# Optimization experiments

Measured on AMD Instinct MI355X. Metric: run time of the kernel, lower is better.

## Reference

```python
import jax, jax.numpy as jnp
import numpy as np

B, L, D, H = 4, 2048, 1024, 16
HD = D // H
EPS = 1e-6
THETA = 10000.0


def _rmsnorm(x, w):
    rms = jax.lax.rsqrt(jnp.mean(x * x, axis=-1, keepdims=True) + EPS)
    return x * rms * w


def _rope(q, k):
    # q,k: [B,H,L,HD]; standard half-split rotary embedding
    pos = jnp.arange(L, dtype=jnp.float32)
    inv_freq = 1.0 / (THETA ** (jnp.arange(0, HD, 2, dtype=jnp.float32) / HD))  # [HD/2]
    ang = pos[:, None] * inv_freq[None, :]                 # [L, HD/2]
    cos = jnp.cos(ang)[None, None]                         # [1,1,L,HD/2]
    sin = jnp.sin(ang)[None, None]

    def rot(t):
        t1, t2 = t[..., : HD // 2], t[..., HD // 2 :]
        return jnp.concatenate([t1 * cos - t2 * sin, t1 * sin + t2 * cos], axis=-1)

    return rot(q), rot(k)


def setup_inputs() -> dict:
    key = jax.random.key(0)
    ks = jax.random.split(key, 4)
    return {
        "x": jax.random.normal(ks[0], (B, L, D), dtype=jnp.float32),
        "Wqkv": jax.random.normal(ks[1], (D, 3 * D), dtype=jnp.float32) * (D ** -0.5),
        "bqkv": jnp.zeros((3 * D,), dtype=jnp.float32),
        "qn_w": jnp.ones((HD,), dtype=jnp.float32),
        "kn_w": jnp.ones((HD,), dtype=jnp.float32),
        "Wout": jax.random.normal(ks[2], (D, D), dtype=jnp.float32) * (D ** -0.5),
        "bout": jnp.zeros((D,), dtype=jnp.float32),
    }


def reference(x, Wqkv, bqkv, qn_w, kn_w, Wout, bout):
    # QKV projection: [B,L,3D] -> [3,B,H,L,HD]
    qkv = (x @ Wqkv + bqkv).reshape(B, L, 3, H, HD).transpose(2, 0, 3, 1, 4)
    q, k, v = qkv[0], qkv[1], qkv[2]
    # QK-RMSNorm over head_dim
    q = _rmsnorm(q, qn_w)
    k = _rmsnorm(k, kn_w)
    # RoPE
    q, k = _rope(q, k)
    # softmax attention
    scale = HD ** -0.5
    attn = jnp.einsum("bhqd,bhkd->bhqk", q, k) * scale
    attn = jax.nn.softmax(attn, axis=-1)
    out = jnp.einsum("bhqk,bhkd->bhqd", attn, v)
    out = out.transpose(0, 2, 1, 3).reshape(B, L, D)
    return out @ Wout + bout
```

## Files before the change

### kernel.cpp

```cpp
#include <hip/hip_runtime.h>
#include <hip/hip_bf16.h>
#include <math.h>


#define NB 4
#define NL 2048
#define ND 1024
#define NH 16
#define NHD 64
#define GM (NB * NL)

typedef _Float16 f16;
typedef _Float16 half4v __attribute__((ext_vector_type(4)));
typedef _Float16 half8v __attribute__((ext_vector_type(8)));
typedef float f32x4 __attribute__((ext_vector_type(4)));

#define MFMA16(a, b, c) __builtin_amdgcn_mfma_f32_16x16x32_f16((a), (b), (c), 0, 0, 0)

__device__ __forceinline__ void gload16(const void* g, void* l) {
  __builtin_amdgcn_global_load_lds((const __attribute__((address_space(1))) void*)g,
                                   (__attribute__((address_space(3))) void*)l, 16, 0, 0);
}

__global__ __launch_bounds__(256) void sctable(float* __restrict__ tbl) {
  const int idx = blockIdx.x * 256 + threadIdx.x;
  const int l = idx >> 5, i = idx & 31;
  const float invf = exp2f(-(float)i * 0.41524101186092029f);
  const float ang = (float)l * invf;
  tbl[idx] = cosf(ang);
  tbl[65536 + idx] = sinf(ang);
}

__global__ __launch_bounds__(256) void transplit(const float* __restrict__ Wsrc,
                                                 f16* __restrict__ Th,
                                                 f16* __restrict__ Tl, int N) {
  __shared__ float t[64][65];
  const int tid = threadIdx.x;
  const int n0 = blockIdx.x * 64, k0 = blockIdx.y * 64;
#pragma unroll
  for (int it = 0; it < 4; ++it) {
    const int e = it * 256 + tid;
    const int r = e >> 4, c4 = (e & 15) << 2;
    const float4 v = *(const float4*)&Wsrc[(size_t)(k0 + r) * N + n0 + c4];
    t[r][c4] = v.x; t[r][c4 + 1] = v.y; t[r][c4 + 2] = v.z; t[r][c4 + 3] = v.w;
  }
  __syncthreads();
#pragma unroll
  for (int it = 0; it < 4; ++it) {
    const int e = it * 256 + tid;
    const int rn = e >> 4, ck = (e & 15) << 2;
    half4v h, lo;
#pragma unroll
    for (int u = 0; u < 4; ++u) {
      const float v = t[ck + u][rn];
      const f16 hv = (f16)v;
      h[u] = hv;
      lo[u] = (f16)(v - (float)hv);
    }
    *(half4v*)&Th[(size_t)(n0 + rn) * 1024 + k0 + ck] = h;
    *(half4v*)&Tl[(size_t)(n0 + rn) * 1024 + k0 + ck] = lo;
  }
}

template <int N, int ASRC, int MODE>
__global__ __launch_bounds__(256) void gemm_split(
    const float* __restrict__ A32, const f16* __restrict__ Ah_g,
    const f16* __restrict__ Al_g, const f16* __restrict__ Bh_g,
    const f16* __restrict__ Bl_g, const float* __restrict__ bias,
    float* __restrict__ out32, f16* __restrict__ qh, f16* __restrict__ ql,
    f16* __restrict__ kh, f16* __restrict__ kl, f16* __restrict__ vth,
    const float* __restrict__ qw, const float* __restrict__ kw,
    const float* __restrict__ tbl) {
  __shared__ f16 Ah[4096], Al[4096], Bh[4096], Bl[4096];
  const int tid = threadIdx.x;
  const int ln = tid & 63, wv = tid >> 6;
  const int ln15 = ln & 15, q4 = ln >> 4;

  const int nwg = (N / 128) * (GM / 128);
  const int flat = blockIdx.y * gridDim.x + blockIdx.x;
  const int sw = (flat & 7) * (nwg >> 3) + (flat >> 3);
  const int bx = sw % (N / 128), by = sw / (N / 128);
  const int m0 = by * 128, n0 = bx * 128;
  const int wr = wv >> 1, wc = wv & 1;

  f32x4 acc[4][4];
#pragma unroll
  for (int i = 0; i < 4; ++i)
#pragma unroll
    for (int j = 0; j < 4; ++j) acc[i][j] = (f32x4){0.f, 0.f, 0.f, 0.f};

  for (int k0 = 0; k0 < 1024; k0 += 32) {
    if constexpr (ASRC == 0) {
#pragma unroll
      for (int it = 0; it < 4; ++it) {
        const int e = it * 256 + tid;
        const int row = e >> 3, kq = (e & 7) << 2;
        const float4 v = *(const float4*)&A32[(size_t)(m0 + row) * 1024 + k0 + kq];
        half4v h, lo;
        h[0] = (f16)v.x; lo[0] = (f16)(v.x - (float)h[0]);
        h[1] = (f16)v.y; lo[1] = (f16)(v.y - (float)h[1]);
        h[2] = (f16)v.z; lo[2] = (f16)(v.z - (float)h[2]);
        h[3] = (f16)v.w; lo[3] = (f16)(v.w - (float)h[3]);
        const int idx = ((row >> 4) << 9) + (((row & 15) + ((kq >> 3) << 4)) << 3) + (kq & 7);
        *(half4v*)&Ah[idx] = h;
        *(half4v*)&Al[idx] = lo;
      }
#pragma unroll
      for (int t = 0; t < 2; ++t) {
        const int f = wv * 2 + t;
        const size_t off = (size_t)(n0 + f * 16 + ln15) * 1024 + k0 + q4 * 8;
        gload16(Bh_g + off, &Bh[f * 512]);
        gload16(Bl_g + off, &Bl[f * 512]);
      }
    } else {
#pragma unroll
      for (int t = 0; t < 2; ++t) {
        const int f = wv * 2 + t;
        const size_t aoff = (size_t)(m0 + f * 16 + ln15) * 1024 + k0 + q4 * 8;
        const size_t boff = (size_t)(n0 + f * 16 + ln15) * 1024 + k0 + q4 * 8;
        gload16(Ah_g + aoff, &Ah[f * 512]);
        gload16(Al_g + aoff, &Al[f * 512]);
        gload16(Bh_g + boff, &Bh[f * 512]);
        gload16(Bl_g + boff, &Bl[f * 512]);
      }
    }
    __syncthreads();

    half8v a_h[4], a_l[4];
#pragma unroll
    for (int i = 0; i < 4; ++i) {
      a_h[i] = *(half8v*)&Ah[(wr * 4 + i) * 512 + ln * 8];
      a_l[i] = *(half8v*)&Al[(wr * 4 + i) * 512 + ln * 8];
    }
#pragma unroll
    for (int j = 0; j < 4; ++j) {
      const half8v b_h = *(half8v*)&Bh[(wc * 4 + j) * 512 + ln * 8];
      const half8v b_l = *(half8v*)&Bl[(wc * 4 + j) * 512 + ln * 8];
#pragma unroll
      for (int i = 0; i < 4; ++i) {
        acc[i][j] = MFMA16(a_h[i], b_h, acc[i][j]);
        acc[i][j] = MFMA16(a_l[i], b_h, acc[i][j]);
        acc[i][j] = MFMA16(a_h[i], b_l, acc[i][j]);
      }
    }
    __syncthreads();
  }

  const int nc = n0 + wc * 64;
  float bv[4];
#pragma unroll
  for (int j = 0; j < 4; ++j) bv[j] = bias[nc + j * 16 + ln15];

  if constexpr (MODE == 0) {
#pragma unroll
    for (int i = 0; i < 4; ++i) {
      const int m = m0 + wr * 64 + i * 16 + q4 * 4;
#pragma unroll
      for (int j = 0; j < 4; ++j)
#pragma unroll
        for (int r = 0; r < 4; ++r)
          out32[(size_t)(m + r) * N + nc + j * 16 + ln15] = acc[i][j][r] + bv[j];
    }
  } else {
    const int s = nc >> 10;
    const int h = (nc >> 6) & 15;
    if (s == 2) {
#pragma unroll
      for (int i = 0; i < 4; ++i) {
        const int m = m0 + wr * 64 + i * 16 + q4 * 4;
        const int b = m >> 11, l0 = m & (NL - 1);
#pragma unroll
        for (int j = 0; j < 4; ++j) {
          half4v pv;
#pragma unroll
          for (int r = 0; r < 4; ++r) pv[r] = (f16)(acc[i][j][r] + bv[j]);
          *(half4v*)&vth[(size_t)((b * NH + h) * NHD + j * 16 + ln15) * NL + l0] = pv;
        }
      }
    } else {
      const float* nw = (s == 0) ? qw : kw;
      f16* dh = (s == 0) ? qh : kh;
      f16* dl = (s == 0) ? ql : kl;
      const float qsc = (s == 0) ? 0.125f * 1.4426950408889634f : 1.0f;
      float wn[4];
#pragma unroll
      for (int j = 0; j < 4; ++j) wn[j] = nw[j * 16 + ln15];
#pragma unroll
      for (int i = 0; i < 4; ++i) {
        const int m = m0 + wr * 64 + i * 16 + q4 * 4;
        const int b = m >> 11, l0 = m & (NL - 1);
        float vv[4][4];
        float ss[4] = {0.f, 0.f, 0.f, 0.f};
#pragma unroll
        for (int j = 0; j < 4; ++j)
#pragma unroll
          for (int r = 0; r < 4; ++r) {
            vv[j][r] = acc[i][j][r] + bv[j];
            ss[r] += vv[j][r] * vv[j][r];
          }
#pragma unroll
        for (int r = 0; r < 4; ++r) {
          ss[r] += __shfl_xor(ss[r], 1);
          ss[r] += __shfl_xor(ss[r], 2);
          ss[r] += __shfl_xor(ss[r], 4);
          ss[r] += __shfl_xor(ss[r], 8);
          ss[r] = rsqrtf(ss[r] * (1.0f / 64.0f) + 1e-6f);
        }
#pragma unroll
        for (int j = 0; j < 4; ++j)
#pragma unroll
          for (int r = 0; r < 4; ++r) vv[j][r] *= ss[r] * wn[j];
#pragma unroll
        for (int jj = 0; jj < 2; ++jj)
#pragma unroll
          for (int r = 0; r < 4; ++r) {
            const int l = l0 + r;
            const float c = tbl[l * 32 + jj * 16 + ln15];
            const float sn = tbl[65536 + l * 32 + jj * 16 + ln15];
            const float t1 = vv[jj][r], t2 = vv[jj + 2][r];
            vv[jj][r] = t1 * c - t2 * sn;
            vv[jj + 2][r] = t1 * sn + t2 * c;
          }
#pragma unroll
        for (int j = 0; j < 4; ++j)
#pragma unroll
          for (int r = 0; r < 4; ++r) {
            const float val = vv[j][r] * qsc;
            const f16 hv = (f16)val;
            const size_t di = (size_t)((b * NH + h) * NL + l0 + r) * NHD + j * 16 + ln15;
            dh[di] = hv;
            dl[di] = (f16)(val - (float)hv);
          }
      }
    }
  }
}

__global__ __launch_bounds__(256) void flash_mfma(
    const f16* __restrict__ qh, const f16* __restrict__ ql,
    const f16* __restrict__ kh, const f16* __restrict__ kl,
    const f16* __restrict__ vth, f16* __restrict__ Oh, f16* __restrict__ Ol) {
  __shared__ f16 KH[4096], KL[4096], VT[4096];
  __shared__ f16 P[4][32][72];
  const int tid = threadIdx.x;
  const int ln = tid & 63, wv = tid >> 6;
  const int ln15 = ln & 15, q4 = ln >> 4;

  const int flat = blockIdx.x;
  const int swz = (flat & 7) * 128 + (flat >> 3);
  const int head = swz >> 4;
  const int qt = swz & 15;
  const int b = head >> 4, h = head & 15;
  const int q0 = qt * 128 + wv * 32;
  const size_t hbase = (size_t)head * NL * NHD;

  half8v qfh[2][2], qfl[2][2];
#pragma unroll
  for (int rf = 0; rf < 2; ++rf)
#pragma unroll
    for (int kb = 0; kb < 2; ++kb) {
      const size_t off = hbase + (size_t)(q0 + rf * 16 + ln15) * NHD + kb * 32 + q4 * 8;
      qfh[rf][kb] = *(const half8v*)&qh[off];
      qfl[rf][kb] = *(const half8v*)&ql[off];
    }

  f32x4 o_[2][4];
  float m_[2][4], l_[2][4];
#pragma unroll
  for (int rf = 0; rf < 2; ++rf)
#pragma unroll
    for (int cf = 0; cf < 4; ++cf) o_[rf][cf] = (f32x4){0.f, 0.f, 0.f, 0.f};
#pragma unroll
  for (int rf = 0; rf < 2; ++rf)
#pragma unroll
    for (int r = 0; r < 4; ++r) {
      m_[rf][r] = -INFINITY;
      l_[rf][r] = 0.f;
    }

  for (int kt = 0; kt < NL / 64; ++kt) {
    const int kv0 = kt * 64;
#pragma unroll
    for (int t = 0; t < 6; ++t) {
      const int f = wv * 6 + t;
      if (f < 8) {
        gload16(kh + hbase + (size_t)(kv0 + (f >> 1) * 16 + ln15) * NHD + (f & 1) * 32 + q4 * 8,
                &KH[f * 512]);
      } else if (f < 16) {
        const int g = f - 8;
        gload16(kl + hbase + (size_t)(kv0 + (g >> 1) * 16 + ln15) * NHD + (g & 1) * 32 + q4 * 8,
                &KL[g * 512]);
      } else {
        const int g = f - 16;
        gload16(vth + (size_t)(head * NHD + (g >> 1) * 16 + ln15) * NL + kv0 + (g & 1) * 32 + q4 * 8,
                &VT[g * 512]);
      }
    }
    __syncthreads();

    f32x4 s_[2][4];
#pragma unroll
    for (int rf = 0; rf < 2; ++rf)
#pragma unroll
      for (int cb = 0; cb < 4; ++cb) s_[rf][cb] = (f32x4){0.f, 0.f, 0.f, 0.f};
#pragma unroll
    for (int cb = 0; cb < 4; ++cb) {
      const half8v kh0 = *(half8v*)&KH[(cb * 2 + 0) * 512 + ln * 8];
      const half8v kh1 = *(half8v*)&KH[(cb * 2 + 1) * 512 + ln * 8];
      const half8v kl0 = *(half8v*)&KL[(cb * 2 + 0) * 512 + ln * 8];
      const half8v kl1 = *(half8v*)&KL[(cb * 2 + 1) * 512 + ln * 8];
#pragma unroll
      for (int rf = 0; rf < 2; ++rf) {
        f32x4 t = s_[rf][cb];
        t = MFMA16(qfh[rf][0], kh0, t);
        t = MFMA16(qfh[rf][1], kh1, t);
        t = MFMA16(qfl[rf][0], kh0, t);
        t = MFMA16(qfl[rf][1], kh1, t);
        t = MFMA16(qfh[rf][0], kl0, t);
        t = MFMA16(qfh[rf][1], kl1, t);
        s_[rf][cb] = t;
      }
    }

#pragma unroll
    for (int rf = 0; rf < 2; ++rf) {
      float al[4];
#pragma unroll
      for (int r = 0; r < 4; ++r) {
        float pm = fmaxf(fmaxf(s_[rf][0][r], s_[rf][1][r]),
                         fmaxf(s_[rf][2][r], s_[rf][3][r]));
        pm = fmaxf(pm, __shfl_xor(pm, 1));
        pm = fmaxf(pm, __shfl_xor(pm, 2));
        pm = fmaxf(pm, __shfl_xor(pm, 4));
        pm = fmaxf(pm, __shfl_xor(pm, 8));
        const float mn = fmaxf(m_[rf][r], pm);
        al[r] = exp2f(m_[rf][r] - mn);
        m_[rf][r] = mn;
      }
      float rs[4] = {0.f, 0.f, 0.f, 0.f};
#pragma unroll
      for (int cb = 0; cb < 4; ++cb)
#pragma unroll
        for (int r = 0; r < 4; ++r) {
          const float p = exp2f(s_[rf][cb][r] - m_[rf][r]);
          rs[r] += p;
          P[wv][rf * 16 + q4 * 4 + r][cb * 16 + ln15] = (f16)p;
        }
#pragma unroll
      for (int r = 0; r < 4; ++r) {
        rs[r] += __shfl_xor(rs[r], 1);
        rs[r] += __shfl_xor(rs[r], 2);
        rs[r] += __shfl_xor(rs[r], 4);
        rs[r] += __shfl_xor(rs[r], 8);
        l_[rf][r] = l_[rf][r] * al[r] + rs[r];
      }
#pragma unroll
      for (int cf = 0; cf < 4; ++cf)
#pragma unroll
        for (int r = 0; r < 4; ++r) o_[rf][cf][r] *= al[r];
    }

#pragma unroll
    for (int kb = 0; kb < 2; ++kb) {
      half8v pa[2];
#pragma unroll
      for (int rf = 0; rf < 2; ++rf)
        pa[rf] = *(half8v*)&P[wv][rf * 16 + ln15][kb * 32 + q4 * 8];
#pragma unroll
      for (int cf = 0; cf < 4; ++cf) {
        const half8v vb = *(half8v*)&VT[(cf * 2 + kb) * 512 + ln * 8];
#pragma unroll
        for (int rf = 0; rf < 2; ++rf) o_[rf][cf] = MFMA16(pa[rf], vb, o_[rf][cf]);
      }
    }
    __syncthreads();
  }

  float inv[2][4];
#pragma unroll
  for (int rf = 0; rf < 2; ++rf)
#pragma unroll
    for (int r = 0; r < 4; ++r) inv[rf][r] = 1.0f / l_[rf][r];
#pragma unroll
  for (int rf = 0; rf < 2; ++rf)
#pragma unroll
    for (int cf = 0; cf < 4; ++cf) {
      const int q = q0 + rf * 16 + q4 * 4;
#pragma unroll
      for (int r = 0; r < 4; ++r) {
        const float val = o_[rf][cf][r] * inv[rf][r];
        const f16 hv = (f16)val;
        const size_t di = (size_t)(b * NL + q + r) * ND + h * 64 + cf * 16 + ln15;
        Oh[di] = hv;
        Ol[di] = (f16)(val - (float)hv);
      }
    }
}

extern "C" void kernel_launch(void* const* d_in, const int* in_sizes, int n_in,
                              void* d_out, int out_size, void* d_ws,
                              size_t ws_size, hipStream_t stream) {
  const float* x = (const float*)d_in[0];
  const float* Wqkv = (const float*)d_in[1];
  const float* bqkv = (const float*)d_in[2];
  const float* qn_w = (const float*)d_in[3];
  const float* kn_w = (const float*)d_in[4];
  const float* Wout = (const float*)d_in[5];
  const float* bout = (const float*)d_in[6];
  float* out = (float*)d_out;

  char* wsb = (char*)d_ws;
  f16* WqTh = (f16*)(wsb);
  f16* WqTl = (f16*)(wsb + (6u << 20));
  f16* Oh = (f16*)(wsb);
  f16* Ol = (f16*)(wsb + (16u << 20));
  f16* WoTh = (f16*)(wsb + (32u << 20));
  f16* WoTl = (f16*)(wsb + (34u << 20));
  float* tbl = (float*)(wsb + (36u << 20));
  f16* qh = (f16*)(wsb + (37u << 20));
  f16* ql = (f16*)(wsb + (53u << 20));
  f16* kh = (f16*)(wsb + (69u << 20));
  f16* kl = (f16*)(wsb + (85u << 20));
  f16* vth = (f16*)(wsb + (101u << 20));

  sctable<<<256, 256, 0, stream>>>(tbl);
  transplit<<<dim3(48, 16), 256, 0, stream>>>(Wqkv, WqTh, WqTl, 3 * ND);
  transplit<<<dim3(16, 16), 256, 0, stream>>>(Wout, WoTh, WoTl, ND);

  gemm_split<3 * ND, 0, 1><<<dim3(24, 64), 256, 0, stream>>>(
      x, nullptr, nullptr, WqTh, WqTl, bqkv, nullptr, qh, ql, kh, kl, vth,
      qn_w, kn_w, tbl);

  flash_mfma<<<1024, 256, 0, stream>>>(qh, ql, kh, kl, vth, Oh, Ol);

  gemm_split<ND, 1, 0><<<dim3(8, 64), 256, 0, stream>>>(
      nullptr, Oh, Ol, WoTh, WoTl, bout, out, nullptr, nullptr, nullptr,
      nullptr, nullptr, nullptr, nullptr, nullptr);
}
```

Baseline: 684.1 us.

## Transpose flash-attention MFMAs, add lazy max rescaling, and pre-split x into fp16 halves

The flash attention kernel now computes S^T (K as the A operand, Q as B), so each lane owns whole query columns. Row max and sum reductions therefore need only two cross-lane shuffles instead of four per row, and O is stored with vectorized half4 writes. It also skips the rescaling of O and l unless the running max grows by more than 8 (log2 units). That saves exp and multiply work at the cost of a wider bound on fp16 P values. Separately, x is split into hi/lo fp16 once in a new prepass, so the QKV GEMM can use direct global-to-LDS loads for A; this adds extra memory traffic for xh and xl, and the workspace layout is reshuffled to fit them.

```diff
diff --git a/kernel.cpp b/kernel.cpp
--- a/kernel.cpp
+++ b/kernel.cpp
@@ -31,6 +31,20 @@
   tbl[65536 + idx] = sinf(ang);
 }
 
+__global__ __launch_bounds__(256) void presplit(const float* __restrict__ x,
+                                                f16* __restrict__ xh,
+                                                f16* __restrict__ xl) {
+  const size_t i = ((size_t)blockIdx.x * 256 + threadIdx.x) * 4;
+  const float4 v = *(const float4*)&x[i];
+  half4v h, lo;
+  h[0] = (f16)v.x; lo[0] = (f16)(v.x - (float)h[0]);
+  h[1] = (f16)v.y; lo[1] = (f16)(v.y - (float)h[1]);
+  h[2] = (f16)v.z; lo[2] = (f16)(v.z - (float)h[2]);
+  h[3] = (f16)v.w; lo[3] = (f16)(v.w - (float)h[3]);
+  *(half4v*)&xh[i] = h;
+  *(half4v*)&xl[i] = lo;
+}
+
 __global__ __launch_bounds__(256) void transplit(const float* __restrict__ Wsrc,
                                                  f16* __restrict__ Th,
                                                  f16* __restrict__ Tl, int N) {
@@ -62,15 +76,14 @@
   }
 }
 
-template <int N, int ASRC, int MODE>
+template <int N, int MODE>
 __global__ __launch_bounds__(256) void gemm_split(
-    const float* __restrict__ A32, const f16* __restrict__ Ah_g,
-    const f16* __restrict__ Al_g, const f16* __restrict__ Bh_g,
-    const f16* __restrict__ Bl_g, const float* __restrict__ bias,
-    float* __restrict__ out32, f16* __restrict__ qh, f16* __restrict__ ql,
-    f16* __restrict__ kh, f16* __restrict__ kl, f16* __restrict__ vth,
-    const float* __restrict__ qw, const float* __restrict__ kw,
-    const float* __restrict__ tbl) {
+    const f16* __restrict__ Ah_g, const f16* __restrict__ Al_g,
+    const f16* __restrict__ Bh_g, const f16* __restrict__ Bl_g,
+    const float* __restrict__ bias, float* __restrict__ out32,
+    f16* __restrict__ qh, f16* __restrict__ ql, f16* __restrict__ kh,
+    f16* __restrict__ kl, f16* __restrict__ vth, const float* __restrict__ qw,
+    const float* __restrict__ kw, const float* __restrict__ tbl) {
   __shared__ f16 Ah[4096], Al[4096], Bh[4096], Bl[4096];
   const int tid = threadIdx.x;
   const int ln = tid & 63, wv = tid >> 6;
@@ -90,39 +103,15 @@
     for (int j = 0; j < 4; ++j) acc[i][j] = (f32x4){0.f, 0.f, 0.f, 0.f};
 
   for (int k0 = 0; k0 < 1024; k0 += 32) {
-    if constexpr (ASRC == 0) {
-#pragma unroll
-      for (int it = 0; it < 4; ++it) {
-        const int e = it * 256 + tid;
-        const int row = e >> 3, kq = (e & 7) << 2;
-        const float4 v = *(const float4*)&A32[(size_t)(m0 + row) * 1024 + k0 + kq];
-        half4v h, lo;
-        h[0] = (f16)v.x; lo[0] = (f16)(v.x - (float)h[0]);
-        h[1] = (f16)v.y; lo[1] = (f16)(v.y - (float)h[1]);
-        h[2] = (f16)v.z; lo[2] = (f16)(v.z - (float)h[2]);
-        h[3] = (f16)v.w; lo[3] = (f16)(v.w - (float)h[3]);
-        const int idx = ((row >> 4) << 9) + (((row & 15) + ((kq >> 3) << 4)) << 3) + (kq & 7);
-        *(half4v*)&Ah[idx] = h;
-        *(half4v*)&Al[idx] = lo;
-      }
-#pragma unroll
-      for (int t = 0; t < 2; ++t) {
-        const int f = wv * 2 + t;
-        const size_t off = (size_t)(n0 + f * 16 + ln15) * 1024 + k0 + q4 * 8;
-        gload16(Bh_g + off, &Bh[f * 512]);
-        gload16(Bl_g + off, &Bl[f * 512]);
-      }
-    } else {
-#pragma unroll
-      for (int t = 0; t < 2; ++t) {
-        const int f = wv * 2 + t;
-        const size_t aoff = (size_t)(m0 + f * 16 + ln15) * 1024 + k0 + q4 * 8;
-        const size_t boff = (size_t)(n0 + f * 16 + ln15) * 1024 + k0 + q4 * 8;
-        gload16(Ah_g + aoff, &Ah[f * 512]);
-        gload16(Al_g + aoff, &Al[f * 512]);
-        gload16(Bh_g + boff, &Bh[f * 512]);
-        gload16(Bl_g + boff, &Bl[f * 512]);
-      }
+#pragma unroll
+    for (int t = 0; t < 2; ++t) {
+      const int f = wv * 2 + t;
+      const size_t aoff = (size_t)(m0 + f * 16 + ln15) * 1024 + k0 + q4 * 8;
+      const size_t boff = (size_t)(n0 + f * 16 + ln15) * 1024 + k0 + q4 * 8;
+      gload16(Ah_g + aoff, &Ah[f * 512]);
+      gload16(Al_g + aoff, &Al[f * 512]);
+      gload16(Bh_g + boff, &Bh[f * 512]);
+      gload16(Bl_g + boff, &Bl[f * 512]);
     }
     __syncthreads();
 
@@ -241,7 +230,7 @@
     const f16* __restrict__ kh, const f16* __restrict__ kl,
     const f16* __restrict__ vth, f16* __restrict__ Oh, f16* __restrict__ Ol) {
   __shared__ f16 KH[4096], KL[4096], VT[4096];
-  __shared__ f16 P[4][32][72];
+  __shared__ f16 Pl[4][16][72];
   const int tid = threadIdx.x;
   const int ln = tid & 63, wv = tid >> 6;
   const int ln15 = ln & 15, q4 = ln >> 4;
@@ -264,19 +253,14 @@
       qfl[rf][kb] = *(const half8v*)&ql[off];
     }
 
-  f32x4 o_[2][4];
-  float m_[2][4], l_[2][4];
-#pragma unroll
-  for (int rf = 0; rf < 2; ++rf)
-#pragma unroll
-    for (int cf = 0; cf < 4; ++cf) o_[rf][cf] = (f32x4){0.f, 0.f, 0.f, 0.f};
-#pragma unroll
-  for (int rf = 0; rf < 2; ++rf)
-#pragma unroll
-    for (int r = 0; r < 4; ++r) {
-      m_[rf][r] = -INFINITY;
-      l_[rf][r] = 0.f;
-    }
+  f32x4 o_[4][2];
+  float m_[2], l_[2];
+#pragma unroll
+  for (int df = 0; df < 4; ++df)
+#pragma unroll
+    for (int rf = 0; rf < 2; ++rf) o_[df][rf] = (f32x4){0.f, 0.f, 0.f, 0.f};
+  m_[0] = m_[1] = -INFINITY;
+  l_[0] = l_[1] = 0.f;
 
   for (int kt = 0; kt < NL / 64; ++kt) {
     const int kv0 = kt * 64;
@@ -312,89 +296,81 @@
 #pragma unroll
       for (int rf = 0; rf < 2; ++rf) {
         f32x4 t = s_[rf][cb];
-        t = MFMA16(qfh[rf][0], kh0, t);
-        t = MFMA16(qfh[rf][1], kh1, t);
-        t = MFMA16(qfl[rf][0], kh0, t);
-        t = MFMA16(qfl[rf][1], kh1, t);
-        t = MFMA16(qfh[rf][0], kl0, t);
-        t = MFMA16(qfh[rf][1], kl1, t);
+        t = MFMA16(kh0, qfh[rf][0], t);
+        t = MFMA16(kh1, qfh[rf][1], t);
+        t = MFMA16(kl0, qfh[rf][0], t);
+        t = MFMA16(kl1, qfh[rf][1], t);
+        t = MFMA16(kh0, qfl[rf][0], t);
+        t = MFMA16(kh1, qfl[rf][1], t);
         s_[rf][cb] = t;
       }
     }
 
 #pragma unroll
     for (int rf = 0; rf < 2; ++rf) {
-      float al[4];
+      float pmax = -INFINITY;
+#pragma unroll
+      for (int cb = 0; cb < 4; ++cb)
+#pragma unroll
+        for (int r = 0; r < 4; ++r) pmax = fmaxf(pmax, s_[rf][cb][r]);
+      pmax = fmaxf(pmax, __shfl_xor(pmax, 16));
+      pmax = fmaxf(pmax, __shfl_xor(pmax, 32));
+      if (!__all(pmax - m_[rf] <= 8.0f)) {
+        const float mn = fmaxf(m_[rf], pmax);
+        const float al = exp2f(m_[rf] - mn);
+        m_[rf] = mn;
+        l_[rf] *= al;
+#pragma unroll
+        for (int df = 0; df < 4; ++df) o_[df][rf] *= al;
+      }
+      float rs = 0.f;
+#pragma unroll
+      for (int cb = 0; cb < 4; ++cb) {
+        half4v pk;
+#pragma unroll
+        for (int r = 0; r < 4; ++r) {
+          const float p = exp2f(s_[rf][cb][r] - m_[rf]);
+          rs += p;
+          pk[r] = (f16)p;
+        }
+        *(half4v*)&Pl[wv][ln15][cb * 16 + q4 * 4] = pk;
+      }
+      rs += __shfl_xor(rs, 16);
+      rs += __shfl_xor(rs, 32);
+      l_[rf] += rs;
+
+#pragma unroll
+      for (int ks = 0; ks < 2; ++ks) {
+        const half8v pb = *(half8v*)&Pl[wv][ln15][ks * 32 + q4 * 8];
+#pragma unroll
+        for (int df = 0; df < 4; ++df) {
+          const half8v vb = *(half8v*)&VT[(df * 2 + ks) * 512 + ln * 8];
+          o_[df][rf] = MFMA16(vb, pb, o_[df][rf]);
+        }
+      }
+    }
+    __syncthreads();
+  }
+
+#pragma unroll
+  for (int rf = 0; rf < 2; ++rf) {
+    const float invl = 1.0f / l_[rf];
+    const int q = q0 + rf * 16 + ln15;
+    const size_t rowb = (size_t)(b * NL + q) * ND + h * 64;
+#pragma unroll
+    for (int df = 0; df < 4; ++df) {
+      half4v oh_, ol_;
 #pragma unroll
       for (int r = 0; r < 4; ++r) {
-        float pm = fmaxf(fmaxf(s_[rf][0][r], s_[rf][1][r]),
-                         fmaxf(s_[rf][2][r], s_[rf][3][r]));
-        pm = fmaxf(pm, __shfl_xor(pm, 1));
-        pm = fmaxf(pm, __shfl_xor(pm, 2));
-        pm = fmaxf(pm, __shfl_xor(pm, 4));
-        pm = fmaxf(pm, __shfl_xor(pm, 8));
-        const float mn = fmaxf(m_[rf][r], pm);
-        al[r] = exp2f(m_[rf][r] - mn);
-        m_[rf][r] = mn;
-      }
-      float rs[4] = {0.f, 0.f, 0.f, 0.f};
-#pragma unroll
-      for (int cb = 0; cb < 4; ++cb)
-#pragma unroll
-        for (int r = 0; r < 4; ++r) {
-          const float p = exp2f(s_[rf][cb][r] - m_[rf][r]);
-          rs[r] += p;
-          P[wv][rf * 16 + q4 * 4 + r][cb * 16 + ln15] = (f16)p;
-        }
-#pragma unroll
-      for (int r = 0; r < 4; ++r) {
-        rs[r] += __shfl_xor(rs[r], 1);
-        rs[r] += __shfl_xor(rs[r], 2);
-        rs[r] += __shfl_xor(rs[r], 4);
-        rs[r] += __shfl_xor(rs[r], 8);
-        l_[rf][r] = l_[rf][r] * al[r] + rs[r];
-      }
-#pragma unroll
-      for (int cf = 0; cf < 4; ++cf)
-#pragma unroll
-        for (int r = 0; r < 4; ++r) o_[rf][cf][r] *= al[r];
-    }
-
-#pragma unroll
-    for (int kb = 0; kb < 2; ++kb) {
-      half8v pa[2];
-#pragma unroll
-      for (int rf = 0; rf < 2; ++rf)
-        pa[rf] = *(half8v*)&P[wv][rf * 16 + ln15][kb * 32 + q4 * 8];
-#pragma unroll
-      for (int cf = 0; cf < 4; ++cf) {
-        const half8v vb = *(half8v*)&VT[(cf * 2 + kb) * 512 + ln * 8];
-#pragma unroll
-        for (int rf = 0; rf < 2; ++rf) o_[rf][cf] = MFMA16(pa[rf], vb, o_[rf][cf]);
-      }
-    }
-    __syncthreads();
-  }
-
-  float inv[2][4];
-#pragma unroll
-  for (int rf = 0; rf < 2; ++rf)
-#pragma unroll
-    for (int r = 0; r < 4; ++r) inv[rf][r] = 1.0f / l_[rf][r];
-#pragma unroll
-  for (int rf = 0; rf < 2; ++rf)
-#pragma unroll
-    for (int cf = 0; cf < 4; ++cf) {
-      const int q = q0 + rf * 16 + q4 * 4;
-#pragma unroll
-      for (int r = 0; r < 4; ++r) {
-        const float val = o_[rf][cf][r] * inv[rf][r];
+        const float val = o_[df][rf][r] * invl;
         const f16 hv = (f16)val;
-        const size_t di = (size_t)(b * NL + q + r) * ND + h * 64 + cf * 16 + ln15;
-        Oh[di] = hv;
-        Ol[di] = (f16)(val - (float)hv);
-      }
-    }
+        oh_[r] = hv;
+        ol_[r] = (f16)(val - (float)hv);
+      }
+      *(half4v*)&Oh[rowb + df * 16 + q4 * 4] = oh_;
+      *(half4v*)&Ol[rowb + df * 16 + q4 * 4] = ol_;
+    }
+  }
 }
 
 extern "C" void kernel_launch(void* const* d_in, const int* in_sizes, int n_in,
@@ -410,30 +386,33 @@
   float* out = (float*)d_out;
 
   char* wsb = (char*)d_ws;
-  f16* WqTh = (f16*)(wsb);
-  f16* WqTl = (f16*)(wsb + (6u << 20));
-  f16* Oh = (f16*)(wsb);
-  f16* Ol = (f16*)(wsb + (16u << 20));
-  f16* WoTh = (f16*)(wsb + (32u << 20));
-  f16* WoTl = (f16*)(wsb + (34u << 20));
-  float* tbl = (float*)(wsb + (36u << 20));
-  f16* qh = (f16*)(wsb + (37u << 20));
-  f16* ql = (f16*)(wsb + (53u << 20));
-  f16* kh = (f16*)(wsb + (69u << 20));
-  f16* kl = (f16*)(wsb + (85u << 20));
-  f16* vth = (f16*)(wsb + (101u << 20));
+  f16* qh = (f16*)(wsb);
+  f16* ql = (f16*)(wsb + (16u << 20));
+  f16* kh = (f16*)(wsb + (32u << 20));
+  f16* kl = (f16*)(wsb + (48u << 20));
+  f16* vth = (f16*)(wsb + (64u << 20));
+  float* tbl = (float*)(wsb + (80u << 20));
+  f16* WqTh = (f16*)(wsb + (81u << 20));
+  f16* WqTl = (f16*)(wsb + (87u << 20));
+  f16* xh = (f16*)(wsb + (93u << 20));
+  f16* xl = (f16*)(wsb + (109u << 20));
+  f16* Oh = (f16*)(wsb + (81u << 20));
+  f16* Ol = (f16*)(wsb + (97u << 20));
+  f16* WoTh = (f16*)(wsb + (113u << 20));
+  f16* WoTl = (f16*)(wsb + (115u << 20));
 
   sctable<<<256, 256, 0, stream>>>(tbl);
   transplit<<<dim3(48, 16), 256, 0, stream>>>(Wqkv, WqTh, WqTl, 3 * ND);
+  presplit<<<8192, 256, 0, stream>>>(x, xh, xl);
+
+  gemm_split<3 * ND, 1><<<dim3(24, 64), 256, 0, stream>>>(
+      xh, xl, WqTh, WqTl, bqkv, nullptr, qh, ql, kh, kl, vth, qn_w, kn_w, tbl);
+
   transplit<<<dim3(16, 16), 256, 0, stream>>>(Wout, WoTh, WoTl, ND);
 
-  gemm_split<3 * ND, 0, 1><<<dim3(24, 64), 256, 0, stream>>>(
-      x, nullptr, nullptr, WqTh, WqTl, bqkv, nullptr, qh, ql, kh, kl, vth,
-      qn_w, kn_w, tbl);
-
   flash_mfma<<<1024, 256, 0, stream>>>(qh, ql, kh, kl, vth, Oh, Ol);
 
-  gemm_split<ND, 1, 0><<<dim3(8, 64), 256, 0, stream>>>(
-      nullptr, Oh, Ol, WoTh, WoTl, bout, out, nullptr, nullptr, nullptr,
-      nullptr, nullptr, nullptr, nullptr, nullptr);
-}
+  gemm_split<ND, 0><<<dim3(8, 64), 256, 0, stream>>>(
+      Oh, Ol, WoTh, WoTl, bout, out, nullptr, nullptr, nullptr, nullptr,
+      nullptr, nullptr, nullptr, nullptr);
+}
```

Result: faster. 567.3 us (-17.1%).
